# Optimization experiments

Hardware: AMD Instinct MI355X
Metric: run time of the kernel (lower is better)

The kernel has to match this reference:

```python
import jax, jax.numpy as jnp
import numpy as np

B, CIN, C, H, W = 8, 256, 128, 128, 128
BN_EPS = 1e-5
EPS = 1e-12


def _bn_params(k, c):
    k1, k2, k3, k4 = jax.random.split(k, 4)
    gamma = jax.random.uniform(k1, (c,), minval=0.5, maxval=1.5)
    beta = jax.random.normal(k2, (c,)) * 0.1
    mean = jax.random.normal(k3, (c,)) * 0.1
    var = jax.random.uniform(k4, (c,), minval=0.5, maxval=1.5)
    return gamma, beta, mean, var


def _xavier(k, cout, cin):
    lim = np.sqrt(6.0 / (cin + cout))
    return jax.random.uniform(k, (cout, cin), minval=-lim, maxval=lim)


def setup_inputs() -> dict:
    key = jax.random.key(0)
    ks = jax.random.split(key, 16)
    inp = {
        'target_task_feats': jax.random.normal(ks[0], (B, CIN, H, W), dtype=jnp.float32),
        'source_task_feats': jax.random.normal(ks[1], (B, CIN, H, W), dtype=jnp.float32),
        'q_w1': _xavier(ks[2], C, CIN), 'q_w2': _xavier(ks[3], C, C),
        'k_w1': _xavier(ks[4], C, CIN), 'k_w2': _xavier(ks[5], C, C),
        'v_w': _xavier(ks[6], C, CIN),
    }
    for name, kk, c in [('q1', ks[7], C), ('q2', ks[8], C), ('k1', ks[9], C), ('k2', ks[10], C), ('v', ks[11], C)]:
        g, b, m, v = _bn_params(kk, c)
        inp[f'{name}_g'], inp[f'{name}_b'], inp[f'{name}_m'], inp[f'{name}_v'] = g, b, m, v
    return inp


def _conv_bn(x, w, g, b, m, v):
    # 1x1 conv (no bias) + eval-mode BatchNorm, fused scale/shift
    y = jnp.einsum('bchw,oc->bohw', x, w)
    scale = (g / jnp.sqrt(v + BN_EPS))[None, :, None, None]
    shift = (b - m * g / jnp.sqrt(v + BN_EPS))[None, :, None, None]
    return y * scale + shift


def reference(target_task_feats, source_task_feats,
              q_w1, q_w2, k_w1, k_w2, v_w,
              q1_g, q1_b, q1_m, q1_v,
              q2_g, q2_b, q2_m, q2_v,
              k1_g, k1_b, k1_m, k1_v,
              k2_g, k2_b, k2_m, k2_v,
              v_g, v_b, v_m, v_v):
    b = target_task_feats.shape[0]
    # key / value from source
    k_h = jax.nn.relu(_conv_bn(source_task_feats, k_w1, k1_g, k1_b, k1_m, k1_v))
    key = jax.nn.softplus(_conv_bn(k_h, k_w2, k2_g, k2_b, k2_m, k2_v)).reshape(b, C, -1)  # [B,C,Ns]
    value = jax.nn.relu(_conv_bn(source_task_feats, v_w, v_g, v_b, v_m, v_v)).reshape(b, C, -1)  # [B,C,Ns]
    # query from target
    q_h = jax.nn.relu(_conv_bn(target_task_feats, q_w1, q1_g, q1_b, q1_m, q1_v))
    query = jax.nn.softplus(_conv_bn(q_h, q_w2, q2_g, q2_b, q2_m, q2_v)).reshape(b, C, -1)  # [B,C,Nt]
    # linear attention: KV^T then Q
    S = jnp.einsum('bcn,bdn->bcd', value, key)      # [B,C,C]
    Z = key.sum(axis=2)                              # [B,C]
    denom = jnp.einsum('bc,bcn->bn', Z, query)[:, None, :]  # [B,1,Nt]
    out = jnp.einsum('bcd,bdn->bcn', S, query) / jnp.maximum(denom, EPS)
    return out.reshape(b, C, H, W)
```

## Files before the change

kernel.cpp:

```cpp
#include <hip/hip_runtime.h>
#include <math.h>

typedef __attribute__((ext_vector_type(8))) short bf8v;
typedef __attribute__((ext_vector_type(4))) float f4v;

#define B_      8
#define CIN_    256
#define C_      128
#define NPIX_   16384
#define EPS_    1e-12f
#define BN_EPS_ 1e-5f

#define OFF_WK1  0u
#define OFF_WV   65536u
#define OFF_WQ1  131072u
#define OFF_WK2  196608u
#define OFF_WQ2  229376u
#define OFF_BIAS 262144u
#define OFF_S    264704u
#define OFF_Z    788992u
#define OFF_SBF  793088u

__device__ __forceinline__ unsigned short f2bf(float f) {
    unsigned u = __float_as_uint(f);
    unsigned r = u + 0x7fffu + ((u >> 16) & 1u);
    return (unsigned short)(r >> 16);
}
__device__ __forceinline__ float lo16(unsigned v){ return __uint_as_float(v << 16); }
__device__ __forceinline__ float hi16(unsigned v){ return __uint_as_float(v & 0xffff0000u); }
__device__ __forceinline__ float softplus_f(float x) {
    return fmaxf(x, 0.f) + __logf(1.f + __expf(-fabsf(x)));
}
__device__ __forceinline__ f4v MFMA(bf8v a, bf8v b, f4v c) {
    return __builtin_amdgcn_mfma_f32_16x16x32_bf16(a, b, c, 0, 0, 0);
}

struct PrepPtrs {
    const float* w[5];
    const float* g[5];
    const float* be[5];
    const float* mu[5];
    const float* va[5];
    unsigned short* wout[5];
    float* bout[5];
};

__global__ void prep_kernel(PrepPtrs p) {
    int idx = blockIdx.x * 256 + threadIdx.x;
    if (idx < 131072) {
        int conv, local, sh;
        if (idx < 32768)       { conv = 0; local = idx;          sh = 8; }
        else if (idx < 65536)  { conv = 1; local = idx - 32768;  sh = 8; }
        else if (idx < 98304)  { conv = 2; local = idx - 65536;  sh = 8; }
        else if (idx < 114688) { conv = 3; local = idx - 98304;  sh = 7; }
        else                   { conv = 4; local = idx - 114688; sh = 7; }
        int o = local >> sh;
        float scale = p.g[conv][o] * rsqrtf(p.va[conv][o] + BN_EPS_);
        p.wout[conv][local] = f2bf(p.w[conv][local] * scale);
    } else if (idx < 131712) {
        int j = idx - 131072;
        int conv = j >> 7;
        int o = j & 127;
        float scale = p.g[conv][o] * rsqrtf(p.va[conv][o] + BN_EPS_);
        p.bout[conv][o] = p.be[conv][o] - p.mu[conv][o] * scale;
    }
}

__global__ __launch_bounds__(256, 2)
void srcS(const float* __restrict__ src,
          const unsigned short* __restrict__ Wk1, const unsigned short* __restrict__ Wv,
          const unsigned short* __restrict__ Wk2, const float* __restrict__ bias,
          float* __restrict__ Sbuf, float* __restrict__ Zbuf)
{
    __shared__ __align__(16) char smem[52224];
    unsigned short* xT = (unsigned short*)smem;
    unsigned short* hT = (unsigned short*)(smem + 33792);
    unsigned short* stgV = xT;
    unsigned short* stgK = hT;

    const int tid = threadIdx.x;
    const int L = tid & 63, w = tid >> 6;
    const int lr = L & 15, qd = L >> 4;
    const int b = blockIdx.y;
    const int m0 = w * 32;
    const int kbq = qd * 8;
    const int m0s = (w & 1) * 64, n0s = (w >> 1) * 64;
    const float* bk1 = bias + 0;
    const float* bvp = bias + 128;
    const float* bk2 = bias + 384;

    f4v zz = {0.f, 0.f, 0.f, 0.f};
    f4v sAcc[4][4];
    #pragma unroll
    for (int mt = 0; mt < 4; mt++)
        #pragma unroll
        for (int nt = 0; nt < 4; nt++) sAcc[mt][nt] = zz;
    float zacc = 0.f;
    const int zc = tid >> 1, zh = tid & 1;

    for (int wd = 0; wd < 4; wd++) {
        const int gn0 = blockIdx.x * 256 + wd * 64;

        #pragma unroll
        for (int s = 0; s < 4; s++) {
            int id = tid + s * 256;
            int n4 = (id & 15) * 4;
            int k0 = (id >> 4) * 4;
            float4 r[4];
            #pragma unroll
            for (int i = 0; i < 4; i++)
                r[i] = *(const float4*)(src + (size_t)(b * 256 + k0 + i) * NPIX_ + gn0 + n4);
            #pragma unroll
            for (int j = 0; j < 4; j++) {
                ushort4 t;
                t.x = f2bf(((const float*)&r[0])[j]);
                t.y = f2bf(((const float*)&r[1])[j]);
                t.z = f2bf(((const float*)&r[2])[j]);
                t.w = f2bf(((const float*)&r[3])[j]);
                *(ushort4*)(xT + (n4 + j) * 264 + k0) = t;
            }
        }
        __syncthreads();

        f4v hAcc[2][4], vAcc[2][4];
        #pragma unroll
        for (int mt = 0; mt < 2; mt++)
            #pragma unroll
            for (int nt = 0; nt < 4; nt++) { hAcc[mt][nt] = zz; vAcc[mt][nt] = zz; }
        #pragma unroll
        for (int ks = 0; ks < 8; ks++) {
            const int kb = ks * 32 + kbq;
            bf8v a1[2], a2[2], bx[4];
            #pragma unroll
            for (int mt = 0; mt < 2; mt++) {
                a1[mt] = *(const bf8v*)(Wk1 + (m0 + mt * 16 + lr) * 256 + kb);
                a2[mt] = *(const bf8v*)(Wv  + (m0 + mt * 16 + lr) * 256 + kb);
            }
            #pragma unroll
            for (int nt = 0; nt < 4; nt++)
                bx[nt] = *(const bf8v*)(xT + (nt * 16 + lr) * 264 + kb);
            #pragma unroll
            for (int mt = 0; mt < 2; mt++)
                #pragma unroll
                for (int nt = 0; nt < 4; nt++) {
                    hAcc[mt][nt] = MFMA(a1[mt], bx[nt], hAcc[mt][nt]);
                    vAcc[mt][nt] = MFMA(a2[mt], bx[nt], vAcc[mt][nt]);
                }
        }
        #pragma unroll
        for (int mt = 0; mt < 2; mt++) {
            const float4 b4 = *(const float4*)(bk1 + m0 + mt * 16 + qd * 4);
            #pragma unroll
            for (int nt = 0; nt < 4; nt++) {
                ushort4 t;
                t.x = f2bf(fmaxf(hAcc[mt][nt][0] + b4.x, 0.f));
                t.y = f2bf(fmaxf(hAcc[mt][nt][1] + b4.y, 0.f));
                t.z = f2bf(fmaxf(hAcc[mt][nt][2] + b4.z, 0.f));
                t.w = f2bf(fmaxf(hAcc[mt][nt][3] + b4.w, 0.f));
                *(ushort4*)(hT + (nt * 16 + lr) * 136 + m0 + mt * 16 + qd * 4) = t;
            }
        }
        __syncthreads();
        #pragma unroll
        for (int mt = 0; mt < 2; mt++) {
            const float4 b4 = *(const float4*)(bvp + m0 + mt * 16 + qd * 4);
            const float* bp = (const float*)&b4;
            #pragma unroll
            for (int nt = 0; nt < 4; nt++)
                #pragma unroll
                for (int r = 0; r < 4; r++)
                    vAcc[mt][nt][r] = fmaxf(vAcc[mt][nt][r] + bp[r], 0.f);
        }

        f4v kAcc[2][4];
        #pragma unroll
        for (int mt = 0; mt < 2; mt++)
            #pragma unroll
            for (int nt = 0; nt < 4; nt++) kAcc[mt][nt] = zz;
        #pragma unroll
        for (int ks = 0; ks < 4; ks++) {
            const int kb = ks * 32 + kbq;
            bf8v a[2], bh[4];
            #pragma unroll
            for (int mt = 0; mt < 2; mt++)
                a[mt] = *(const bf8v*)(Wk2 + (m0 + mt * 16 + lr) * 128 + kb);
            #pragma unroll
            for (int nt = 0; nt < 4; nt++)
                bh[nt] = *(const bf8v*)(hT + (nt * 16 + lr) * 136 + kb);
            #pragma unroll
            for (int mt = 0; mt < 2; mt++)
                #pragma unroll
                for (int nt = 0; nt < 4; nt++)
                    kAcc[mt][nt] = MFMA(a[mt], bh[nt], kAcc[mt][nt]);
        }
        __syncthreads();

        #pragma unroll
        for (int mt = 0; mt < 2; mt++) {
            const float4 b4 = *(const float4*)(bk2 + m0 + mt * 16 + qd * 4);
            const float* bp = (const float*)&b4;
            #pragma unroll
            for (int nt = 0; nt < 4; nt++)
                #pragma unroll
                for (int r = 0; r < 4; r++) {
                    int m = m0 + mt * 16 + qd * 4 + r;
                    stgV[m * 72 + nt * 16 + lr] = f2bf(vAcc[mt][nt][r]);
                    stgK[m * 72 + nt * 16 + lr] = f2bf(softplus_f(kAcc[mt][nt][r] + bp[r]));
                }
        }
        __syncthreads();

        {
            const unsigned short* kr = stgK + zc * 72 + zh * 32;
            #pragma unroll
            for (int p = 0; p < 4; p++) {
                uint4 t = *(const uint4*)(kr + p * 8);
                zacc += lo16(t.x) + hi16(t.x) + lo16(t.y) + hi16(t.y)
                      + lo16(t.z) + hi16(t.z) + lo16(t.w) + hi16(t.w);
            }
        }
        #pragma unroll
        for (int kk = 0; kk < 2; kk++) {
            const int kb = kk * 32 + kbq;
            bf8v a[4], bb[4];
            #pragma unroll
            for (int mt = 0; mt < 4; mt++)
                a[mt] = *(const bf8v*)(stgV + (m0s + mt * 16 + lr) * 72 + kb);
            #pragma unroll
            for (int nt = 0; nt < 4; nt++)
                bb[nt] = *(const bf8v*)(stgK + (n0s + nt * 16 + lr) * 72 + kb);
            #pragma unroll
            for (int mt = 0; mt < 4; mt++)
                #pragma unroll
                for (int nt = 0; nt < 4; nt++)
                    sAcc[mt][nt] = MFMA(a[mt], bb[nt], sAcc[mt][nt]);
        }
        __syncthreads();
    }

    #pragma unroll
    for (int mt = 0; mt < 4; mt++)
        #pragma unroll
        for (int nt = 0; nt < 4; nt++)
            #pragma unroll
            for (int r = 0; r < 4; r++) {
                int m = m0s + mt * 16 + qd * 4 + r;
                int cN = n0s + nt * 16 + lr;
                atomicAdd(Sbuf + ((size_t)b * 128 + m) * 128 + cN, sAcc[mt][nt][r]);
            }
    atomicAdd(Zbuf + b * 128 + zc, zacc);
}

__global__ void cvts(const float* __restrict__ Sbuf, unsigned short* __restrict__ Sbf) {
    int i = blockIdx.x * 256 + threadIdx.x;
    if (i < 131072) Sbf[i] = f2bf(Sbuf[i]);
}

__global__ __launch_bounds__(256)
void tgtAttn(const float* __restrict__ tgt,
             const unsigned short* __restrict__ Wq1, const unsigned short* __restrict__ Wq2,
             const float* __restrict__ bias, const unsigned short* __restrict__ Sbf,
             const float* __restrict__ Zbuf, float* __restrict__ out)
{
    __shared__ __align__(16) char smem[51968];
    unsigned short* xT = (unsigned short*)smem;
    unsigned short* qT = (unsigned short*)(smem + 33792);
    float* dn  = (float*)(smem + 33792 + 17408);
    float* Zsh = dn + 64;

    const int tid = threadIdx.x;
    const int L = tid & 63, w = tid >> 6;
    const int lr = L & 15, qd = L >> 4;
    const int b = blockIdx.y;
    const int gn0 = blockIdx.x * 64;
    const int m0 = w * 32;
    const int kbq = qd * 8;
    const float* bq1 = bias + 256;
    const float* bq2 = bias + 512;

    if (tid < 128) Zsh[tid] = Zbuf[b * 128 + tid];
    #pragma unroll
    for (int s = 0; s < 4; s++) {
        int id = tid + s * 256;
        int n4 = (id & 15) * 4;
        int k0 = (id >> 4) * 4;
        float4 r[4];
        #pragma unroll
        for (int i = 0; i < 4; i++)
            r[i] = *(const float4*)(tgt + (size_t)(b * 256 + k0 + i) * NPIX_ + gn0 + n4);
        #pragma unroll
        for (int j = 0; j < 4; j++) {
            ushort4 t;
            t.x = f2bf(((const float*)&r[0])[j]);
            t.y = f2bf(((const float*)&r[1])[j]);
            t.z = f2bf(((const float*)&r[2])[j]);
            t.w = f2bf(((const float*)&r[3])[j]);
            *(ushort4*)(xT + (n4 + j) * 264 + k0) = t;
        }
    }
    __syncthreads();

    f4v zz = {0.f, 0.f, 0.f, 0.f};
    f4v acc1[2][4];
    #pragma unroll
    for (int mt = 0; mt < 2; mt++)
        #pragma unroll
        for (int nt = 0; nt < 4; nt++) acc1[mt][nt] = zz;
    #pragma unroll
    for (int ks = 0; ks < 8; ks++) {
        const int kb = ks * 32 + kbq;
        bf8v a[2], bx[4];
        #pragma unroll
        for (int mt = 0; mt < 2; mt++)
            a[mt] = *(const bf8v*)(Wq1 + (m0 + mt * 16 + lr) * 256 + kb);
        #pragma unroll
        for (int nt = 0; nt < 4; nt++)
            bx[nt] = *(const bf8v*)(xT + (nt * 16 + lr) * 264 + kb);
        #pragma unroll
        for (int mt = 0; mt < 2; mt++)
            #pragma unroll
            for (int nt = 0; nt < 4; nt++)
                acc1[mt][nt] = MFMA(a[mt], bx[nt], acc1[mt][nt]);
    }
    #pragma unroll
    for (int mt = 0; mt < 2; mt++) {
        const float4 b4 = *(const float4*)(bq1 + m0 + mt * 16 + qd * 4);
        #pragma unroll
        for (int nt = 0; nt < 4; nt++) {
            ushort4 t;
            t.x = f2bf(fmaxf(acc1[mt][nt][0] + b4.x, 0.f));
            t.y = f2bf(fmaxf(acc1[mt][nt][1] + b4.y, 0.f));
            t.z = f2bf(fmaxf(acc1[mt][nt][2] + b4.z, 0.f));
            t.w = f2bf(fmaxf(acc1[mt][nt][3] + b4.w, 0.f));
            *(ushort4*)(qT + (nt * 16 + lr) * 136 + m0 + mt * 16 + qd * 4) = t;
        }
    }
    __syncthreads();

    f4v acc2[2][4];
    #pragma unroll
    for (int mt = 0; mt < 2; mt++)
        #pragma unroll
        for (int nt = 0; nt < 4; nt++) acc2[mt][nt] = zz;
    #pragma unroll
    for (int ks = 0; ks < 4; ks++) {
        const int kb = ks * 32 + kbq;
        bf8v a[2], bh[4];
        #pragma unroll
        for (int mt = 0; mt < 2; mt++)
            a[mt] = *(const bf8v*)(Wq2 + (m0 + mt * 16 + lr) * 128 + kb);
        #pragma unroll
        for (int nt = 0; nt < 4; nt++)
            bh[nt] = *(const bf8v*)(qT + (nt * 16 + lr) * 136 + kb);
        #pragma unroll
        for (int mt = 0; mt < 2; mt++)
            #pragma unroll
            for (int nt = 0; nt < 4; nt++)
                acc2[mt][nt] = MFMA(a[mt], bh[nt], acc2[mt][nt]);
    }
    __syncthreads();
    #pragma unroll
    for (int mt = 0; mt < 2; mt++) {
        const float4 b4 = *(const float4*)(bq2 + m0 + mt * 16 + qd * 4);
        const float* bp = (const float*)&b4;
        #pragma unroll
        for (int nt = 0; nt < 4; nt++) {
            ushort4 t;
            t.x = f2bf(softplus_f(acc2[mt][nt][0] + bp[0]));
            t.y = f2bf(softplus_f(acc2[mt][nt][1] + bp[1]));
            t.z = f2bf(softplus_f(acc2[mt][nt][2] + bp[2]));
            t.w = f2bf(softplus_f(acc2[mt][nt][3] + bp[3]));
            *(ushort4*)(qT + (nt * 16 + lr) * 136 + m0 + mt * 16 + qd * 4) = t;
        }
    }
    __syncthreads();

    if (tid < 64) {
        const unsigned short* qr = qT + tid * 136;
        float s = 0.f;
        #pragma unroll
        for (int d = 0; d < 128; d += 8) {
            uint4 t = *(const uint4*)(qr + d);
            s = fmaf(Zsh[d + 0], lo16(t.x), s);
            s = fmaf(Zsh[d + 1], hi16(t.x), s);
            s = fmaf(Zsh[d + 2], lo16(t.y), s);
            s = fmaf(Zsh[d + 3], hi16(t.y), s);
            s = fmaf(Zsh[d + 4], lo16(t.z), s);
            s = fmaf(Zsh[d + 5], hi16(t.z), s);
            s = fmaf(Zsh[d + 6], lo16(t.w), s);
            s = fmaf(Zsh[d + 7], hi16(t.w), s);
        }
        dn[tid] = fmaxf(s, EPS_);
    }

    f4v oacc[2][4];
    #pragma unroll
    for (int mt = 0; mt < 2; mt++)
        #pragma unroll
        for (int nt = 0; nt < 4; nt++) oacc[mt][nt] = zz;
    #pragma unroll
    for (int ks = 0; ks < 4; ks++) {
        const int kb = ks * 32 + kbq;
        bf8v a[2], bq[4];
        #pragma unroll
        for (int mt = 0; mt < 2; mt++)
            a[mt] = *(const bf8v*)(Sbf + (size_t)b * 16384 + (m0 + mt * 16 + lr) * 128 + kb);
        #pragma unroll
        for (int nt = 0; nt < 4; nt++)
            bq[nt] = *(const bf8v*)(qT + (nt * 16 + lr) * 136 + kb);
        #pragma unroll
        for (int mt = 0; mt < 2; mt++)
            #pragma unroll
            for (int nt = 0; nt < 4; nt++)
                oacc[mt][nt] = MFMA(a[mt], bq[nt], oacc[mt][nt]);
    }
    __syncthreads();

    float inv[4];
    #pragma unroll
    for (int nt = 0; nt < 4; nt++) inv[nt] = 1.f / dn[nt * 16 + lr];
    #pragma unroll
    for (int mt = 0; mt < 2; mt++)
        #pragma unroll
        for (int nt = 0; nt < 4; nt++)
            #pragma unroll
            for (int r = 0; r < 4; r++) {
                int m = m0 + mt * 16 + qd * 4 + r;
                out[(size_t)(b * 128 + m) * NPIX_ + gn0 + nt * 16 + lr] = oacc[mt][nt][r] * inv[nt];
            }
}

extern "C" void kernel_launch(void* const* d_in, const int* in_sizes, int n_in,
                              void* d_out, int out_size, void* d_ws, size_t ws_size,
                              hipStream_t stream)
{
    const float* tgt = (const float*)d_in[0];
    const float* src = (const float*)d_in[1];
    char* ws = (char*)d_ws;
    unsigned short* Wk1 = (unsigned short*)(ws + OFF_WK1);
    unsigned short* Wv  = (unsigned short*)(ws + OFF_WV);
    unsigned short* Wq1 = (unsigned short*)(ws + OFF_WQ1);
    unsigned short* Wk2 = (unsigned short*)(ws + OFF_WK2);
    unsigned short* Wq2 = (unsigned short*)(ws + OFF_WQ2);
    float* bias = (float*)(ws + OFF_BIAS);
    float* Sbuf = (float*)(ws + OFF_S);
    float* Zbuf = (float*)(ws + OFF_Z);
    unsigned short* Sbf = (unsigned short*)(ws + OFF_SBF);

    PrepPtrs p;
    p.w[0] = (const float*)d_in[4];
    p.w[1] = (const float*)d_in[6];
    p.w[2] = (const float*)d_in[2];
    p.w[3] = (const float*)d_in[5];
    p.w[4] = (const float*)d_in[3];
    const int gbase[5] = {15, 23, 7, 19, 11};
    for (int c = 0; c < 5; c++) {
        p.g[c]  = (const float*)d_in[gbase[c]];
        p.be[c] = (const float*)d_in[gbase[c] + 1];
        p.mu[c] = (const float*)d_in[gbase[c] + 2];
        p.va[c] = (const float*)d_in[gbase[c] + 3];
    }
    p.wout[0] = Wk1; p.wout[1] = Wv; p.wout[2] = Wq1; p.wout[3] = Wk2; p.wout[4] = Wq2;
    p.bout[0] = bias; p.bout[1] = bias + 128; p.bout[2] = bias + 256;
    p.bout[3] = bias + 384; p.bout[4] = bias + 512;

    hipMemsetAsync(ws + OFF_S, 0, 524288 + 4096, stream);
    hipLaunchKernelGGL(prep_kernel, dim3(515), dim3(256), 0, stream, p);
    hipLaunchKernelGGL(srcS, dim3(64, 8), dim3(256), 0, stream,
                       src, Wk1, Wv, Wk2, bias, Sbuf, Zbuf);
    hipLaunchKernelGGL(cvts, dim3(512), dim3(256), 0, stream, Sbuf, Sbf);
    hipLaunchKernelGGL(tgtAttn, dim3(256, 8), dim3(256), 0, stream,
                       tgt, Wq1, Wq2, bias, Sbf, Zbuf, (float*)d_out);
}
```

Measured before the change: 483.6 us.

## Prefetch next pixel tile into registers during MFMA work in srcS and tgtAttn

In srcS, the source tile for the next 64-pixel window is now loaded from global memory into registers (split into two halves) while the current window's MFMA stages run. It is converted to bf16 into shared memory only after the current tile is consumed. tgtAttn now processes two 64-pixel windows per block with the second window prefetched the same way, halving its grid and adding launch_bounds occupancy hint 2. This aims to hide global load latency behind compute, at the cost of many extra registers (up to 64 floats of prefetch) that may lower occupancy or cause spills.

```diff
diff --git a/kernel.cpp b/kernel.cpp
--- a/kernel.cpp
+++ b/kernel.cpp
@@ -88,6 +88,7 @@
     const float* bk1 = bias + 0;
     const float* bvp = bias + 128;
     const float* bk2 = bias + 384;
+    const int gn0b = blockIdx.x * 256;
 
     f4v zz = {0.f, 0.f, 0.f, 0.f};
     f4v sAcc[4][4];
@@ -98,29 +99,43 @@
     float zacc = 0.f;
     const int zc = tid >> 1, zh = tid & 1;
 
+    #pragma unroll
+    for (int s = 0; s < 4; s++) {
+        int id = tid + s * 256;
+        int n4 = (id & 15) * 4;
+        int k0 = (id >> 4) * 4;
+        float4 r[4];
+        #pragma unroll
+        for (int i = 0; i < 4; i++)
+            r[i] = *(const float4*)(src + (size_t)(b * 256 + k0 + i) * NPIX_ + gn0b + n4);
+        #pragma unroll
+        for (int j = 0; j < 4; j++) {
+            ushort4 t;
+            t.x = f2bf(((const float*)&r[0])[j]);
+            t.y = f2bf(((const float*)&r[1])[j]);
+            t.z = f2bf(((const float*)&r[2])[j]);
+            t.w = f2bf(((const float*)&r[3])[j]);
+            *(ushort4*)(xT + (n4 + j) * 264 + k0) = t;
+        }
+    }
+    __syncthreads();
+
+    float4 pfA[8], pfB[8];
+
     for (int wd = 0; wd < 4; wd++) {
-        const int gn0 = blockIdx.x * 256 + wd * 64;
-
-        #pragma unroll
-        for (int s = 0; s < 4; s++) {
-            int id = tid + s * 256;
-            int n4 = (id & 15) * 4;
-            int k0 = (id >> 4) * 4;
-            float4 r[4];
-            #pragma unroll
-            for (int i = 0; i < 4; i++)
-                r[i] = *(const float4*)(src + (size_t)(b * 256 + k0 + i) * NPIX_ + gn0 + n4);
-            #pragma unroll
-            for (int j = 0; j < 4; j++) {
-                ushort4 t;
-                t.x = f2bf(((const float*)&r[0])[j]);
-                t.y = f2bf(((const float*)&r[1])[j]);
-                t.z = f2bf(((const float*)&r[2])[j]);
-                t.w = f2bf(((const float*)&r[3])[j]);
-                *(ushort4*)(xT + (n4 + j) * 264 + k0) = t;
-            }
-        }
-        __syncthreads();
+        const int gn1 = gn0b + (wd + 1) * 64;
+
+        if (wd < 3) {
+            #pragma unroll
+            for (int s = 0; s < 2; s++) {
+                int id = tid + s * 256;
+                int n4 = (id & 15) * 4;
+                int k0 = (id >> 4) * 4;
+                #pragma unroll
+                for (int i = 0; i < 4; i++)
+                    pfA[s * 4 + i] = *(const float4*)(src + (size_t)(b * 256 + k0 + i) * NPIX_ + gn1 + n4);
+            }
+        }
 
         f4v hAcc[2][4], vAcc[2][4];
         #pragma unroll
@@ -161,6 +176,19 @@
             }
         }
         __syncthreads();
+
+        if (wd < 3) {
+            #pragma unroll
+            for (int s = 0; s < 2; s++) {
+                int id = tid + (s + 2) * 256;
+                int n4 = (id & 15) * 4;
+                int k0 = (id >> 4) * 4;
+                #pragma unroll
+                for (int i = 0; i < 4; i++)
+                    pfB[s * 4 + i] = *(const float4*)(src + (size_t)(b * 256 + k0 + i) * NPIX_ + gn1 + n4);
+            }
+        }
+
         #pragma unroll
         for (int mt = 0; mt < 2; mt++) {
             const float4 b4 = *(const float4*)(bvp + m0 + mt * 16 + qd * 4);
@@ -236,6 +264,26 @@
                     sAcc[mt][nt] = MFMA(a[mt], bb[nt], sAcc[mt][nt]);
         }
         __syncthreads();
+
+        if (wd < 3) {
+            #pragma unroll
+            for (int s = 0; s < 4; s++) {
+                int id = tid + s * 256;
+                int n4 = (id & 15) * 4;
+                int k0 = (id >> 4) * 4;
+                const float4* r = (s < 2) ? (pfA + s * 4) : (pfB + (s - 2) * 4);
+                #pragma unroll
+                for (int j = 0; j < 4; j++) {
+                    ushort4 t;
+                    t.x = f2bf(((const float*)&r[0])[j]);
+                    t.y = f2bf(((const float*)&r[1])[j]);
+                    t.z = f2bf(((const float*)&r[2])[j]);
+                    t.w = f2bf(((const float*)&r[3])[j]);
+                    *(ushort4*)(xT + (n4 + j) * 264 + k0) = t;
+                }
+            }
+            __syncthreads();
+        }
     }
 
     #pragma unroll
@@ -256,7 +304,7 @@
     if (i < 131072) Sbf[i] = f2bf(Sbuf[i]);
 }
 
-__global__ __launch_bounds__(256)
+__global__ __launch_bounds__(256, 2)
 void tgtAttn(const float* __restrict__ tgt,
              const unsigned short* __restrict__ Wq1, const unsigned short* __restrict__ Wq2,
              const float* __restrict__ bias, const unsigned short* __restrict__ Sbf,
@@ -272,13 +320,14 @@
     const int L = tid & 63, w = tid >> 6;
     const int lr = L & 15, qd = L >> 4;
     const int b = blockIdx.y;
-    const int gn0 = blockIdx.x * 64;
+    const int gnb = blockIdx.x * 128;
     const int m0 = w * 32;
     const int kbq = qd * 8;
     const float* bq1 = bias + 256;
     const float* bq2 = bias + 512;
 
     if (tid < 128) Zsh[tid] = Zbuf[b * 128 + tid];
+
     #pragma unroll
     for (int s = 0; s < 4; s++) {
         int id = tid + s * 256;
@@ -287,7 +336,7 @@
         float4 r[4];
         #pragma unroll
         for (int i = 0; i < 4; i++)
-            r[i] = *(const float4*)(tgt + (size_t)(b * 256 + k0 + i) * NPIX_ + gn0 + n4);
+            r[i] = *(const float4*)(tgt + (size_t)(b * 256 + k0 + i) * NPIX_ + gnb + n4);
         #pragma unroll
         for (int j = 0; j < 4; j++) {
             ushort4 t;
@@ -300,134 +349,171 @@
     }
     __syncthreads();
 
+    float4 pf[16];
     f4v zz = {0.f, 0.f, 0.f, 0.f};
-    f4v acc1[2][4];
-    #pragma unroll
-    for (int mt = 0; mt < 2; mt++)
-        #pragma unroll
-        for (int nt = 0; nt < 4; nt++) acc1[mt][nt] = zz;
-    #pragma unroll
-    for (int ks = 0; ks < 8; ks++) {
-        const int kb = ks * 32 + kbq;
-        bf8v a[2], bx[4];
+
+    for (int wd = 0; wd < 2; wd++) {
+        const int gn0 = gnb + wd * 64;
+
+        if (wd == 0) {
+            #pragma unroll
+            for (int s = 0; s < 4; s++) {
+                int id = tid + s * 256;
+                int n4 = (id & 15) * 4;
+                int k0 = (id >> 4) * 4;
+                #pragma unroll
+                for (int i = 0; i < 4; i++)
+                    pf[s * 4 + i] = *(const float4*)(tgt + (size_t)(b * 256 + k0 + i) * NPIX_ + gnb + 64 + n4);
+            }
+        }
+
+        f4v acc1[2][4];
         #pragma unroll
         for (int mt = 0; mt < 2; mt++)
-            a[mt] = *(const bf8v*)(Wq1 + (m0 + mt * 16 + lr) * 256 + kb);
-        #pragma unroll
-        for (int nt = 0; nt < 4; nt++)
-            bx[nt] = *(const bf8v*)(xT + (nt * 16 + lr) * 264 + kb);
+            #pragma unroll
+            for (int nt = 0; nt < 4; nt++) acc1[mt][nt] = zz;
+        #pragma unroll
+        for (int ks = 0; ks < 8; ks++) {
+            const int kb = ks * 32 + kbq;
+            bf8v a[2], bx[4];
+            #pragma unroll
+            for (int mt = 0; mt < 2; mt++)
+                a[mt] = *(const bf8v*)(Wq1 + (m0 + mt * 16 + lr) * 256 + kb);
+            #pragma unroll
+            for (int nt = 0; nt < 4; nt++)
+                bx[nt] = *(const bf8v*)(xT + (nt * 16 + lr) * 264 + kb);
+            #pragma unroll
+            for (int mt = 0; mt < 2; mt++)
+                #pragma unroll
+                for (int nt = 0; nt < 4; nt++)
+                    acc1[mt][nt] = MFMA(a[mt], bx[nt], acc1[mt][nt]);
+        }
+        #pragma unroll
+        for (int mt = 0; mt < 2; mt++) {
+            const float4 b4 = *(const float4*)(bq1 + m0 + mt * 16 + qd * 4);
+            #pragma unroll
+            for (int nt = 0; nt < 4; nt++) {
+                ushort4 t;
+                t.x = f2bf(fmaxf(acc1[mt][nt][0] + b4.x, 0.f));
+                t.y = f2bf(fmaxf(acc1[mt][nt][1] + b4.y, 0.f));
+                t.z = f2bf(fmaxf(acc1[mt][nt][2] + b4.z, 0.f));
+                t.w = f2bf(fmaxf(acc1[mt][nt][3] + b4.w, 0.f));
+                *(ushort4*)(qT + (nt * 16 + lr) * 136 + m0 + mt * 16 + qd * 4) = t;
+            }
+        }
+        __syncthreads();
+
+        if (wd == 0) {
+            #pragma unroll
+            for (int s = 0; s < 4; s++) {
+                int id = tid + s * 256;
+                int n4 = (id & 15) * 4;
+                int k0 = (id >> 4) * 4;
+                const float4* r = pf + s * 4;
+                #pragma unroll
+                for (int j = 0; j < 4; j++) {
+                    ushort4 t;
+                    t.x = f2bf(((const float*)&r[0])[j]);
+                    t.y = f2bf(((const float*)&r[1])[j]);
+                    t.z = f2bf(((const float*)&r[2])[j]);
+                    t.w = f2bf(((const float*)&r[3])[j]);
+                    *(ushort4*)(xT + (n4 + j) * 264 + k0) = t;
+                }
+            }
+        }
+
+        f4v acc2[2][4];
         #pragma unroll
         for (int mt = 0; mt < 2; mt++)
             #pragma unroll
-            for (int nt = 0; nt < 4; nt++)
-                acc1[mt][nt] = MFMA(a[mt], bx[nt], acc1[mt][nt]);
+            for (int nt = 0; nt < 4; nt++) acc2[mt][nt] = zz;
+        #pragma unroll
+        for (int ks = 0; ks < 4; ks++) {
+            const int kb = ks * 32 + kbq;
+            bf8v a[2], bh[4];
+            #pragma unroll
+            for (int mt = 0; mt < 2; mt++)
+                a[mt] = *(const bf8v*)(Wq2 + (m0 + mt * 16 + lr) * 128 + kb);
+            #pragma unroll
+            for (int nt = 0; nt < 4; nt++)
+                bh[nt] = *(const bf8v*)(qT + (nt * 16 + lr) * 136 + kb);
+            #pragma unroll
+            for (int mt = 0; mt < 2; mt++)
+                #pragma unroll
+                for (int nt = 0; nt < 4; nt++)
+                    acc2[mt][nt] = MFMA(a[mt], bh[nt], acc2[mt][nt]);
+        }
+        __syncthreads();
+        #pragma unroll
+        for (int mt = 0; mt < 2; mt++) {
+            const float4 b4 = *(const float4*)(bq2 + m0 + mt * 16 + qd * 4);
+            const float* bp = (const float*)&b4;
+            #pragma unroll
+            for (int nt = 0; nt < 4; nt++) {
+                ushort4 t;
+                t.x = f2bf(softplus_f(acc2[mt][nt][0] + bp[0]));
+                t.y = f2bf(softplus_f(acc2[mt][nt][1] + bp[1]));
+                t.z = f2bf(softplus_f(acc2[mt][nt][2] + bp[2]));
+                t.w = f2bf(softplus_f(acc2[mt][nt][3] + bp[3]));
+                *(ushort4*)(qT + (nt * 16 + lr) * 136 + m0 + mt * 16 + qd * 4) = t;
+            }
+        }
+        __syncthreads();
+
+        if (tid < 64) {
+            const unsigned short* qr = qT + tid * 136;
+            float s = 0.f;
+            #pragma unroll
+            for (int d = 0; d < 128; d += 8) {
+                uint4 t = *(const uint4*)(qr + d);
+                s = fmaf(Zsh[d + 0], lo16(t.x), s);
+                s = fmaf(Zsh[d + 1], hi16(t.x), s);
+                s = fmaf(Zsh[d + 2], lo16(t.y), s);
+                s = fmaf(Zsh[d + 3], hi16(t.y), s);
+                s = fmaf(Zsh[d + 4], lo16(t.z), s);
+                s = fmaf(Zsh[d + 5], hi16(t.z), s);
+                s = fmaf(Zsh[d + 6], lo16(t.w), s);
+                s = fmaf(Zsh[d + 7], hi16(t.w), s);
+            }
+            dn[tid] = fmaxf(s, EPS_);
+        }
+
+        f4v oacc[2][4];
+        #pragma unroll
+        for (int mt = 0; mt < 2; mt++)
+            #pragma unroll
+            for (int nt = 0; nt < 4; nt++) oacc[mt][nt] = zz;
+        #pragma unroll
+        for (int ks = 0; ks < 4; ks++) {
+            const int kb = ks * 32 + kbq;
+            bf8v a[2], bq[4];
+            #pragma unroll
+            for (int mt = 0; mt < 2; mt++)
+                a[mt] = *(const bf8v*)(Sbf + (size_t)b * 16384 + (m0 + mt * 16 + lr) * 128 + kb);
+            #pragma unroll
+            for (int nt = 0; nt < 4; nt++)
+                bq[nt] = *(const bf8v*)(qT + (nt * 16 + lr) * 136 + kb);
+            #pragma unroll
+            for (int mt = 0; mt < 2; mt++)
+                #pragma unroll
+                for (int nt = 0; nt < 4; nt++)
+                    oacc[mt][nt] = MFMA(a[mt], bq[nt], oacc[mt][nt]);
+        }
+        __syncthreads();
+
+        float inv[4];
+        #pragma unroll
+        for (int nt = 0; nt < 4; nt++) inv[nt] = 1.f / dn[nt * 16 + lr];
+        #pragma unroll
+        for (int mt = 0; mt < 2; mt++)
+            #pragma unroll
+            for (int nt = 0; nt < 4; nt++)
+                #pragma unroll
+                for (int r = 0; r < 4; r++) {
+                    int m = m0 + mt * 16 + qd * 4 + r;
+                    out[(size_t)(b * 128 + m) * NPIX_ + gn0 + nt * 16 + lr] = oacc[mt][nt][r] * inv[nt];
+                }
     }
-    #pragma unroll
-    for (int mt = 0; mt < 2; mt++) {
-        const float4 b4 = *(const float4*)(bq1 + m0 + mt * 16 + qd * 4);
-        #pragma unroll
-        for (int nt = 0; nt < 4; nt++) {
-            ushort4 t;
-            t.x = f2bf(fmaxf(acc1[mt][nt][0] + b4.x, 0.f));
-            t.y = f2bf(fmaxf(acc1[mt][nt][1] + b4.y, 0.f));
-            t.z = f2bf(fmaxf(acc1[mt][nt][2] + b4.z, 0.f));
-            t.w = f2bf(fmaxf(acc1[mt][nt][3] + b4.w, 0.f));
-            *(ushort4*)(qT + (nt * 16 + lr) * 136 + m0 + mt * 16 + qd * 4) = t;
-        }
-    }
-    __syncthreads();
-
-    f4v acc2[2][4];
-    #pragma unroll
-    for (int mt = 0; mt < 2; mt++)
-        #pragma unroll
-        for (int nt = 0; nt < 4; nt++) acc2[mt][nt] = zz;
-    #pragma unroll
-    for (int ks = 0; ks < 4; ks++) {
-        const int kb = ks * 32 + kbq;
-        bf8v a[2], bh[4];
-        #pragma unroll
-        for (int mt = 0; mt < 2; mt++)
-            a[mt] = *(const bf8v*)(Wq2 + (m0 + mt * 16 + lr) * 128 + kb);
-        #pragma unroll
-        for (int nt = 0; nt < 4; nt++)
-            bh[nt] = *(const bf8v*)(qT + (nt * 16 + lr) * 136 + kb);
-        #pragma unroll
-        for (int mt = 0; mt < 2; mt++)
-            #pragma unroll
-            for (int nt = 0; nt < 4; nt++)
-                acc2[mt][nt] = MFMA(a[mt], bh[nt], acc2[mt][nt]);
-    }
-    __syncthreads();
-    #pragma unroll
-    for (int mt = 0; mt < 2; mt++) {
-        const float4 b4 = *(const float4*)(bq2 + m0 + mt * 16 + qd * 4);
-        const float* bp = (const float*)&b4;
-        #pragma unroll
-        for (int nt = 0; nt < 4; nt++) {
-            ushort4 t;
-            t.x = f2bf(softplus_f(acc2[mt][nt][0] + bp[0]));
-            t.y = f2bf(softplus_f(acc2[mt][nt][1] + bp[1]));
-            t.z = f2bf(softplus_f(acc2[mt][nt][2] + bp[2]));
-            t.w = f2bf(softplus_f(acc2[mt][nt][3] + bp[3]));
-            *(ushort4*)(qT + (nt * 16 + lr) * 136 + m0 + mt * 16 + qd * 4) = t;
-        }
-    }
-    __syncthreads();
-
-    if (tid < 64) {
-        const unsigned short* qr = qT + tid * 136;
-        float s = 0.f;
-        #pragma unroll
-        for (int d = 0; d < 128; d += 8) {
-            uint4 t = *(const uint4*)(qr + d);
-            s = fmaf(Zsh[d + 0], lo16(t.x), s);
-            s = fmaf(Zsh[d + 1], hi16(t.x), s);
-            s = fmaf(Zsh[d + 2], lo16(t.y), s);
-            s = fmaf(Zsh[d + 3], hi16(t.y), s);
-            s = fmaf(Zsh[d + 4], lo16(t.z), s);
-            s = fmaf(Zsh[d + 5], hi16(t.z), s);
-            s = fmaf(Zsh[d + 6], lo16(t.w), s);
-            s = fmaf(Zsh[d + 7], hi16(t.w), s);
-        }
-        dn[tid] = fmaxf(s, EPS_);
-    }
-
-    f4v oacc[2][4];
-    #pragma unroll
-    for (int mt = 0; mt < 2; mt++)
-        #pragma unroll
-        for (int nt = 0; nt < 4; nt++) oacc[mt][nt] = zz;
-    #pragma unroll
-    for (int ks = 0; ks < 4; ks++) {
-        const int kb = ks * 32 + kbq;
-        bf8v a[2], bq[4];
-        #pragma unroll
-        for (int mt = 0; mt < 2; mt++)
-            a[mt] = *(const bf8v*)(Sbf + (size_t)b * 16384 + (m0 + mt * 16 + lr) * 128 + kb);
-        #pragma unroll
-        for (int nt = 0; nt < 4; nt++)
-            bq[nt] = *(const bf8v*)(qT + (nt * 16 + lr) * 136 + kb);
-        #pragma unroll
-        for (int mt = 0; mt < 2; mt++)
-            #pragma unroll
-            for (int nt = 0; nt < 4; nt++)
-                oacc[mt][nt] = MFMA(a[mt], bq[nt], oacc[mt][nt]);
-    }
-    __syncthreads();
-
-    float inv[4];
-    #pragma unroll
-    for (int nt = 0; nt < 4; nt++) inv[nt] = 1.f / dn[nt * 16 + lr];
-    #pragma unroll
-    for (int mt = 0; mt < 2; mt++)
-        #pragma unroll
-        for (int nt = 0; nt < 4; nt++)
-            #pragma unroll
-            for (int r = 0; r < 4; r++) {
-                int m = m0 + mt * 16 + qd * 4 + r;
-                out[(size_t)(b * 128 + m) * NPIX_ + gn0 + nt * 16 + lr] = oacc[mt][nt][r] * inv[nt];
-            }
 }
 
 extern "C" void kernel_launch(void* const* d_in, const int* in_sizes, int n_in,
@@ -469,6 +555,6 @@
     hipLaunchKernelGGL(srcS, dim3(64, 8), dim3(256), 0, stream,
                        src, Wk1, Wv, Wk2, bias, Sbuf, Zbuf);
     hipLaunchKernelGGL(cvts, dim3(512), dim3(256), 0, stream, Sbuf, Sbf);
-    hipLaunchKernelGGL(tgtAttn, dim3(256, 8), dim3(256), 0, stream,
+    hipLaunchKernelGGL(tgtAttn, dim3(128, 8), dim3(256), 0, stream,
                        tgt, Wq1, Wq2, bias, Sbf, Zbuf, (float*)d_out);
 }
```

Result: slower. 613.0 us (+26.7%).
